# Kernel optimization log

Measured on AMD Instinct MI355X. Metric: run time of the kernel, lower is better.

Reference implementation:

```python
import jax, jax.numpy as jnp
import numpy as np

N_NODES = 100000
N_EDGES = 1600000
DIM = 32  # size_in


def setup_inputs() -> dict:
    key = jax.random.key(0)
    k = jax.random.split(key, 8)
    N, E, D = N_NODES, N_EDGES, DIM
    x = jax.random.normal(k[0], (N, 2 * D), dtype=jnp.float32)
    edge_index = jax.random.randint(k[1], (2, E), 0, N, dtype=jnp.int64)
    # Glorot-ish scaled weights (PyG GCNConv uses glorot init); biases zero.
    W1 = jax.random.normal(k[2], (2 * D, 2 * D), dtype=jnp.float32) * (1.0 / np.sqrt(2 * D))
    b1 = jnp.zeros((2 * D,), dtype=jnp.float32)
    W2 = jax.random.normal(k[3], (2 * D, D), dtype=jnp.float32) * (1.0 / np.sqrt(2 * D))
    b2 = jnp.zeros((D,), dtype=jnp.float32)
    W3 = jax.random.normal(k[4], (D, 1), dtype=jnp.float32) * (1.0 / np.sqrt(D))
    b3 = jnp.zeros((1,), dtype=jnp.float32)
    return {"x": x, "edge_index": edge_index, "W1": W1, "b1": b1,
            "W2": W2, "b2": b2, "W3": W3, "b3": b3}


def _gcn_norm(edge_index, num_nodes):
    # PyG gcn_norm with add_self_loops=True, edge_weight=1:
    # deg[i] = # incoming edges (incl. self loop); norm_e = deg[src]^-1/2 * deg[dst]^-1/2
    loop = jnp.arange(num_nodes, dtype=edge_index.dtype)
    src = jnp.concatenate([edge_index[0], loop])
    dst = jnp.concatenate([edge_index[1], loop])
    ones = jnp.ones(src.shape[0], dtype=jnp.float32)
    deg = jax.ops.segment_sum(ones, dst, num_segments=num_nodes)
    dis = jnp.where(deg > 0, jax.lax.rsqrt(deg), 0.0)
    norm = dis[src] * dis[dst]
    return src, dst, norm


def _gcn_conv(h, W, b, src, dst, norm, num_nodes):
    # linear transform first (PyG order), then normalized scatter-add aggregation
    h = h @ W  # [N, out]
    msg = h[src] * norm[:, None]  # gather over edges
    agg = jax.ops.segment_sum(msg, dst, num_segments=num_nodes)
    return agg + b


def reference(x, edge_index, W1, b1, W2, b2, W3, b3):
    N = x.shape[0]
    src, dst, norm = _gcn_norm(edge_index, N)
    out = jnp.tanh(_gcn_conv(x, W1, b1, src, dst, norm, N))
    out = jnp.tanh(_gcn_conv(out, W2, b2, src, dst, norm, N))
    out = _gcn_conv(out, W3, b3, src, dst, norm, N)
    return out
```

## Files before the change

### kernel.cpp

```cpp
#include <hip/hip_runtime.h>
#include <hip/hip_fp16.h>
#include <math.h>

static constexpr int NN = 100000;
static constexpr int NE = 1600000;
static constexpr int BUCK_SH = 5;
static constexpr int NBUK = NN >> BUCK_SH;
static constexpr int NCH = 256;
static constexpr int CH = NE / NCH;

__global__ __launch_bounds__(256)
void k_chist(const int* __restrict__ ei, int* __restrict__ H) {
  __shared__ int h[NBUK];
  for (int i = threadIdx.x; i < NBUK; i += 256) h[i] = 0;
  __syncthreads();
  int chunk = blockIdx.x;
  int start = chunk * CH;
  for (int e = start + threadIdx.x; e < start + CH; e += 256)
    atomicAdd(&h[ei[NE + e] >> BUCK_SH], 1);
  __syncthreads();
  int* Hc = H + chunk * NBUK;
  for (int i = threadIdx.x; i < NBUK; i += 256) Hc[i] = h[i];
}

__global__ void k_csum(int* __restrict__ H, int* __restrict__ tot) {
  int b = blockIdx.x * blockDim.x + threadIdx.x;
  if (b >= NBUK) return;
  int acc = 0;
#pragma unroll 4
  for (int c = 0; c < NCH; ++c) {
    int v = H[c * NBUK + b];
    H[c * NBUK + b] = acc;
    acc += v;
  }
  tot[b] = acc;
}

__global__ __launch_bounds__(1024)
void k_bscan(const int* __restrict__ tot, int* __restrict__ boff) {
  __shared__ int buf[1024];
  __shared__ int s_carry;
  int tid = threadIdx.x;
  if (tid == 0) s_carry = 0;
  __syncthreads();
  for (int base = 0; base < NBUK; base += 1024) {
    int i = base + tid;
    int v = (i < NBUK) ? tot[i] : 0;
    buf[tid] = v;
    __syncthreads();
#pragma unroll
    for (int off = 1; off < 1024; off <<= 1) {
      int t = (tid >= off) ? buf[tid - off] : 0;
      __syncthreads();
      buf[tid] += t;
      __syncthreads();
    }
    int excl = buf[tid] - v;
    int carry = s_carry;
    if (i < NBUK) boff[i] = carry + excl;
    __syncthreads();
    if (tid == 1023) s_carry = carry + buf[1023];
    __syncthreads();
  }
  if (tid == 0) boff[NBUK] = s_carry;
}

__global__ __launch_bounds__(1024)
void k_scat(const int* __restrict__ ei, const int* __restrict__ H,
            const int* __restrict__ boff, unsigned* __restrict__ se) {
  __shared__ int cur[NBUK];
  int chunk = blockIdx.x;
  const int* Hc = H + chunk * NBUK;
  for (int i = threadIdx.x; i < NBUK; i += 1024) cur[i] = boff[i] + Hc[i];
  __syncthreads();
  int start = chunk * CH;
  for (int e = start + threadIdx.x; e < start + CH; e += 1024) {
    int src = ei[e], dst = ei[NE + e];
    int pos = atomicAdd(&cur[dst >> BUCK_SH], 1);
    se[pos] = ((unsigned)(dst & 31) << 20) | (unsigned)src;
  }
}

__global__ __launch_bounds__(256)
void k_blocal(const unsigned* __restrict__ se, const int* __restrict__ boff,
              int* __restrict__ rowptr, float* __restrict__ dis, int* __restrict__ csr_src) {
  int b = blockIdx.x;
  int base = boff[b], end = boff[b + 1];
  __shared__ int cnt[32], off[32];
  int tid = threadIdx.x;
  if (tid < 32) cnt[tid] = 0;
  __syncthreads();
  for (int k = base + tid; k < end; k += 256)
    atomicAdd(&cnt[se[k] >> 20], 1);
  __syncthreads();
  if (tid == 0) {
    int acc = 0;
#pragma unroll
    for (int i = 0; i < 32; ++i) { off[i] = acc; acc += cnt[i]; }
  }
  __syncthreads();
  if (tid < 32) {
    int node = (b << BUCK_SH) + tid;
    rowptr[node] = base + off[tid];
    dis[node] = rsqrtf(1.0f + (float)cnt[tid]);
    cnt[tid] = 0;
  }
  if (b == 0 && tid == 64) rowptr[NN] = NE;
  __syncthreads();
  for (int k = base + tid; k < end; k += 256) {
    unsigned e = se[k];
    int dl = e >> 20;
    int pos = base + off[dl] + atomicAdd(&cnt[dl], 1);
    csr_src[pos] = (int)(e & 0xFFFFFu);
  }
}

__global__ __launch_bounds__(256)
void k_gemm64_h(const float* __restrict__ in, const float* __restrict__ W,
                const float* __restrict__ dis, __half* __restrict__ g) {
  __shared__ float rows[16 * 64];
  int c = threadIdx.x & 63;
  int wid = threadIdx.x >> 6;
  float Wc[64];
#pragma unroll
  for (int k = 0; k < 64; ++k) Wc[k] = W[k * 64 + c];
  int tiles = NN / 16;
  for (int t = blockIdx.x; t < tiles; t += gridDim.x) {
    int row0 = t * 16;
    __syncthreads();
    ((float4*)rows)[threadIdx.x] = ((const float4*)(in + (size_t)row0 * 64))[threadIdx.x];
    __syncthreads();
#pragma unroll
    for (int r = 0; r < 4; ++r) {
      const float* rp = rows + (wid * 4 + r) * 64;
      float acc = 0.f;
#pragma unroll
      for (int kc = 0; kc < 64; kc += 4) {
        float4 v = *(const float4*)(rp + kc);
        acc = fmaf(v.x, Wc[kc + 0], acc);
        acc = fmaf(v.y, Wc[kc + 1], acc);
        acc = fmaf(v.z, Wc[kc + 2], acc);
        acc = fmaf(v.w, Wc[kc + 3], acc);
      }
      int row = row0 + wid * 4 + r;
      g[row * 64 + c] = __float2half(acc * dis[row]);
    }
  }
}

__device__ __forceinline__ float fast_tanh(float x) {
  float e = __expf(2.0f * x);
  return 1.0f - 2.0f / (e + 1.0f);
}

__device__ __forceinline__ void upadd8(float4 r, float4& lo, float4& hi) {
  __half2* h = (__half2*)&r;
  float2 f0 = __half22float2(h[0]);
  float2 f1 = __half22float2(h[1]);
  float2 f2 = __half22float2(h[2]);
  float2 f3 = __half22float2(h[3]);
  lo.x += f0.x; lo.y += f0.y; lo.z += f1.x; lo.w += f1.y;
  hi.x += f2.x; hi.y += f2.y; hi.z += f3.x; hi.w += f3.y;
}

__global__ __launch_bounds__(256)
void k_agg64f(const int* __restrict__ rowptr, const int* __restrict__ csr_src,
              const __half* __restrict__ g, const float* __restrict__ dis,
              const float* __restrict__ b, const float* __restrict__ W2,
              __half* __restrict__ g2) {
  __shared__ float tile[4][8][68];
  int lane = threadIdx.x & 63;
  int wid = threadIdx.x >> 6;
  int grp = lane >> 3;
  int cl = lane & 7;
  int node = blockIdx.x * 32 + wid * 8 + grp;

  int c2 = lane & 31;
  int ksub = lane >> 5;
  float Wc[32];
#pragma unroll
  for (int k = 0; k < 32; ++k) Wc[k] = W2[(ksub * 32 + k) * 32 + c2];

  const char* base = (const char*)g;
  float4 l0 = {0,0,0,0}, h0 = {0,0,0,0}, l1 = {0,0,0,0}, h1 = {0,0,0,0};
  float4 l2 = {0,0,0,0}, h2 = {0,0,0,0}, l3 = {0,0,0,0}, h3 = {0,0,0,0};
  {
    float4 r = *(const float4*)(base + (size_t)node * 128 + cl * 16);
    upadd8(r, l0, h0);
  }
  int k = rowptr[node], end = rowptr[node + 1];
  for (; k + 4 <= end; k += 4) {
    int s0 = csr_src[k], s1 = csr_src[k + 1], s2 = csr_src[k + 2], s3 = csr_src[k + 3];
    float4 r0 = *(const float4*)(base + (size_t)s0 * 128 + cl * 16);
    float4 r1 = *(const float4*)(base + (size_t)s1 * 128 + cl * 16);
    float4 r2 = *(const float4*)(base + (size_t)s2 * 128 + cl * 16);
    float4 r3 = *(const float4*)(base + (size_t)s3 * 128 + cl * 16);
    upadd8(r0, l0, h0); upadd8(r1, l1, h1);
    upadd8(r2, l2, h2); upadd8(r3, l3, h3);
  }
  for (; k < end; ++k) {
    float4 r = *(const float4*)(base + (size_t)csr_src[k] * 128 + cl * 16);
    upadd8(r, l0, h0);
  }
  float d = dis[node];
  float4 blo = *(const float4*)(b + cl * 8);
  float4 bhi = *(const float4*)(b + cl * 8 + 4);
  float4 vl, vh;
  vl.x = ((l0.x + l1.x) + (l2.x + l3.x)) * d + blo.x;
  vl.y = ((l0.y + l1.y) + (l2.y + l3.y)) * d + blo.y;
  vl.z = ((l0.z + l1.z) + (l2.z + l3.z)) * d + blo.z;
  vl.w = ((l0.w + l1.w) + (l2.w + l3.w)) * d + blo.w;
  vh.x = ((h0.x + h1.x) + (h2.x + h3.x)) * d + bhi.x;
  vh.y = ((h0.y + h1.y) + (h2.y + h3.y)) * d + bhi.y;
  vh.z = ((h0.z + h1.z) + (h2.z + h3.z)) * d + bhi.z;
  vh.w = ((h0.w + h1.w) + (h2.w + h3.w)) * d + bhi.w;
  vl.x = fast_tanh(vl.x); vl.y = fast_tanh(vl.y);
  vl.z = fast_tanh(vl.z); vl.w = fast_tanh(vl.w);
  vh.x = fast_tanh(vh.x); vh.y = fast_tanh(vh.y);
  vh.z = fast_tanh(vh.z); vh.w = fast_tanh(vh.w);

  *(float4*)&tile[wid][grp][cl * 8] = vl;
  *(float4*)&tile[wid][grp][cl * 8 + 4] = vh;

  int rbase = blockIdx.x * 32 + wid * 8;
#pragma unroll
  for (int r = 0; r < 8; ++r) {
    const float* rp = &tile[wid][r][ksub * 32];
    float acc = 0.f;
#pragma unroll
    for (int kc = 0; kc < 32; kc += 4) {
      float4 v = *(const float4*)(rp + kc);
      acc = fmaf(v.x, Wc[kc + 0], acc);
      acc = fmaf(v.y, Wc[kc + 1], acc);
      acc = fmaf(v.z, Wc[kc + 2], acc);
      acc = fmaf(v.w, Wc[kc + 3], acc);
    }
    acc += __shfl_down(acc, 32);
    int row = rbase + r;
    if (ksub == 0) g2[row * 32 + c2] = __float2half(acc * dis[row]);
  }
}

__global__ __launch_bounds__(256)
void k_agg32v(const int* __restrict__ rowptr, const int* __restrict__ csr_src,
              const __half* __restrict__ g, const float* __restrict__ dis,
              const float* __restrict__ b, const float* __restrict__ W3,
              float* __restrict__ Af) {
  int lane = threadIdx.x & 63;
  int grp = lane >> 3;
  int cl = lane & 7;
  int node = blockIdx.x * 32 + (threadIdx.x >> 6) * 8 + grp;
  if (node >= NN) return;
  const char* base = (const char*)g;
  float4 a0 = {0,0,0,0}, a1 = {0,0,0,0}, a2 = {0,0,0,0}, a3 = {0,0,0,0};
  {
    float2 r = *(const float2*)(base + (size_t)node * 64 + cl * 8);
    __half2* h = (__half2*)&r;
    float2 f0 = __half22float2(h[0]), f1 = __half22float2(h[1]);
    a0.x += f0.x; a0.y += f0.y; a0.z += f1.x; a0.w += f1.y;
  }
  int k = rowptr[node], end = rowptr[node + 1];
  for (; k + 8 <= end; k += 8) {
    float2 r0 = *(const float2*)(base + (size_t)csr_src[k + 0] * 64 + cl * 8);
    float2 r1 = *(const float2*)(base + (size_t)csr_src[k + 1] * 64 + cl * 8);
    float2 r2 = *(const float2*)(base + (size_t)csr_src[k + 2] * 64 + cl * 8);
    float2 r3 = *(const float2*)(base + (size_t)csr_src[k + 3] * 64 + cl * 8);
    float2 r4 = *(const float2*)(base + (size_t)csr_src[k + 4] * 64 + cl * 8);
    float2 r5 = *(const float2*)(base + (size_t)csr_src[k + 5] * 64 + cl * 8);
    float2 r6 = *(const float2*)(base + (size_t)csr_src[k + 6] * 64 + cl * 8);
    float2 r7 = *(const float2*)(base + (size_t)csr_src[k + 7] * 64 + cl * 8);
    __half2* h; float2 f;
    h = (__half2*)&r0; f = __half22float2(h[0]); a0.x += f.x; a0.y += f.y;
    f = __half22float2(h[1]); a0.z += f.x; a0.w += f.y;
    h = (__half2*)&r1; f = __half22float2(h[0]); a1.x += f.x; a1.y += f.y;
    f = __half22float2(h[1]); a1.z += f.x; a1.w += f.y;
    h = (__half2*)&r2; f = __half22float2(h[0]); a2.x += f.x; a2.y += f.y;
    f = __half22float2(h[1]); a2.z += f.x; a2.w += f.y;
    h = (__half2*)&r3; f = __half22float2(h[0]); a3.x += f.x; a3.y += f.y;
    f = __half22float2(h[1]); a3.z += f.x; a3.w += f.y;
    h = (__half2*)&r4; f = __half22float2(h[0]); a0.x += f.x; a0.y += f.y;
    f = __half22float2(h[1]); a0.z += f.x; a0.w += f.y;
    h = (__half2*)&r5; f = __half22float2(h[0]); a1.x += f.x; a1.y += f.y;
    f = __half22float2(h[1]); a1.z += f.x; a1.w += f.y;
    h = (__half2*)&r6; f = __half22float2(h[0]); a2.x += f.x; a2.y += f.y;
    f = __half22float2(h[1]); a2.z += f.x; a2.w += f.y;
    h = (__half2*)&r7; f = __half22float2(h[0]); a3.x += f.x; a3.y += f.y;
    f = __half22float2(h[1]); a3.z += f.x; a3.w += f.y;
  }
  for (; k + 4 <= end; k += 4) {
    float2 r0 = *(const float2*)(base + (size_t)csr_src[k + 0] * 64 + cl * 8);
    float2 r1 = *(const float2*)(base + (size_t)csr_src[k + 1] * 64 + cl * 8);
    float2 r2 = *(const float2*)(base + (size_t)csr_src[k + 2] * 64 + cl * 8);
    float2 r3 = *(const float2*)(base + (size_t)csr_src[k + 3] * 64 + cl * 8);
    __half2* h; float2 f;
    h = (__half2*)&r0; f = __half22float2(h[0]); a0.x += f.x; a0.y += f.y;
    f = __half22float2(h[1]); a0.z += f.x; a0.w += f.y;
    h = (__half2*)&r1; f = __half22float2(h[0]); a1.x += f.x; a1.y += f.y;
    f = __half22float2(h[1]); a1.z += f.x; a1.w += f.y;
    h = (__half2*)&r2; f = __half22float2(h[0]); a2.x += f.x; a2.y += f.y;
    f = __half22float2(h[1]); a2.z += f.x; a2.w += f.y;
    h = (__half2*)&r3; f = __half22float2(h[0]); a3.x += f.x; a3.y += f.y;
    f = __half22float2(h[1]); a3.z += f.x; a3.w += f.y;
  }
  for (; k < end; ++k) {
    float2 r = *(const float2*)(base + (size_t)csr_src[k] * 64 + cl * 8);
    __half2* h = (__half2*)&r;
    float2 f0 = __half22float2(h[0]), f1 = __half22float2(h[1]);
    a0.x += f0.x; a0.y += f0.y; a0.z += f1.x; a0.w += f1.y;
  }
  float d = dis[node];
  float4 bb = *(const float4*)(b + cl * 4);
  float4 v;
  v.x = ((a0.x + a1.x) + (a2.x + a3.x)) * d + bb.x;
  v.y = ((a0.y + a1.y) + (a2.y + a3.y)) * d + bb.y;
  v.z = ((a0.z + a1.z) + (a2.z + a3.z)) * d + bb.z;
  v.w = ((a0.w + a1.w) + (a2.w + a3.w)) * d + bb.w;
  v.x = fast_tanh(v.x); v.y = fast_tanh(v.y);
  v.z = fast_tanh(v.z); v.w = fast_tanh(v.w);
  float4 w3 = *(const float4*)(W3 + cl * 4);
  float p = v.x * w3.x + v.y * w3.y + v.z * w3.z + v.w * w3.w;
  p += __shfl_xor(p, 1);
  p += __shfl_xor(p, 2);
  p += __shfl_xor(p, 4);
  if (cl == 0) Af[node] = p * d;
}

__global__ void k_agg1(const int* __restrict__ rowptr, const int* __restrict__ csr_src,
                       const float* __restrict__ g, const float* __restrict__ dis,
                       const float* __restrict__ b, float* __restrict__ out) {
  int node = blockIdx.x * blockDim.x + threadIdx.x;
  if (node >= NN) return;
  float a0 = g[node], a1 = 0.f, a2 = 0.f, a3 = 0.f;
  int beg = rowptr[node], end = rowptr[node + 1];
  int k = beg;
  for (; k + 4 <= end; k += 4) {
    float m0 = g[csr_src[k]], m1 = g[csr_src[k + 1]];
    float m2 = g[csr_src[k + 2]], m3 = g[csr_src[k + 3]];
    a0 += m0; a1 += m1; a2 += m2; a3 += m3;
  }
  for (; k < end; ++k) a0 += g[csr_src[k]];
  out[node] = ((a0 + a1) + (a2 + a3)) * dis[node] + b[0];
}

extern "C" void kernel_launch(void* const* d_in, const int* in_sizes, int n_in,
                              void* d_out, int out_size, void* d_ws, size_t ws_size,
                              hipStream_t stream) {
  const float* x  = (const float*)d_in[0];
  const int*   ei = (const int*)d_in[1];
  const float* W1 = (const float*)d_in[2];
  const float* b1 = (const float*)d_in[3];
  const float* W2 = (const float*)d_in[4];
  const float* b2 = (const float*)d_in[5];
  const float* W3 = (const float*)d_in[6];
  const float* b3 = (const float*)d_in[7];
  float* out = (float*)d_out;

  char* ws = (char*)d_ws;
  int*      H       = (int*)ws;      ws += (size_t)NCH * NBUK * 4;
  int*      tot     = (int*)ws;      ws += ((NBUK + 255)/256)*256 * 4;
  int*      boff    = (int*)ws;      ws += ((NBUK + 1 + 255)/256)*256 * 4;
  unsigned* se      = (unsigned*)ws; ws += (size_t)NE * 4;
  int*      rowptr  = (int*)ws;      ws += ((NN + 1 + 255)/256)*256 * 4;
  int*      csr_src = (int*)ws;      ws += (size_t)NE * 4;
  float*    dis     = (float*)ws;    ws += ((NN + 255)/256)*256 * 4;
  __half*   Ah      = (__half*)ws;   ws += (size_t)NN * 64 * 2;
  __half*   Ah2     = (__half*)ws;   ws += (size_t)NN * 32 * 2;
  float*    Af      = (float*)ws;    ws += (size_t)NN * 4;

  k_chist <<<NCH, 256, 0, stream>>>(ei, H);
  k_csum  <<<(NBUK + 255) / 256, 256, 0, stream>>>(H, tot);
  k_bscan <<<1, 1024, 0, stream>>>(tot, boff);
  k_scat  <<<NCH, 1024, 0, stream>>>(ei, H, boff, se);
  k_blocal<<<NBUK, 256, 0, stream>>>(se, boff, rowptr, dis, csr_src);

  k_gemm64_h<<<1250, 256, 0, stream>>>(x, W1, dis, Ah);
  k_agg64f<<<NN / 32, 256, 0, stream>>>(rowptr, csr_src, Ah, dis, b1, W2, Ah2);
  k_agg32v<<<NN / 32, 256, 0, stream>>>(rowptr, csr_src, Ah2, dis, b2, W3, Af);
  k_agg1<<<(NN + 255) / 256, 256, 0, stream>>>(rowptr, csr_src, Af, dis, b3, out);
}
```

Baseline: 252.0 us.

## Sort nodes by in-degree and process aggregation kernels in degree order

Builds a degree histogram in k_blocal, scans it, and scatters node ids into a degree-sorted permutation. The three aggregation kernels then process nodes through this permutation, so the 8 nodes sharing a wavefront have similar edge counts. This targets load imbalance and divergence inside a wavefront in the gather loops. The cost is two extra small kernels plus an atomic scatter, and output writes and row accesses are no longer contiguous in node order, which loses locality on rowptr, dis and the output stores.

```diff
diff --git a/kernel.cpp b/kernel.cpp
--- a/kernel.cpp
+++ b/kernel.cpp
@@ -10,8 +10,9 @@
 static constexpr int CH = NE / NCH;
 
 __global__ __launch_bounds__(256)
-void k_chist(const int* __restrict__ ei, int* __restrict__ H) {
+void k_chist(const int* __restrict__ ei, int* __restrict__ H, int* __restrict__ dh) {
   __shared__ int h[NBUK];
+  if (blockIdx.x == 0) dh[threadIdx.x] = 0;
   for (int i = threadIdx.x; i < NBUK; i += 256) h[i] = 0;
   __syncthreads();
   int chunk = blockIdx.x;
@@ -83,7 +84,8 @@
 
 __global__ __launch_bounds__(256)
 void k_blocal(const unsigned* __restrict__ se, const int* __restrict__ boff,
-              int* __restrict__ rowptr, float* __restrict__ dis, int* __restrict__ csr_src) {
+              int* __restrict__ rowptr, float* __restrict__ dis, int* __restrict__ csr_src,
+              int* __restrict__ deg, int* __restrict__ dh) {
   int b = blockIdx.x;
   int base = boff[b], end = boff[b + 1];
   __shared__ int cnt[32], off[32];
@@ -103,6 +105,9 @@
     int node = (b << BUCK_SH) + tid;
     rowptr[node] = base + off[tid];
     dis[node] = rsqrtf(1.0f + (float)cnt[tid]);
+    int d = cnt[tid] > 255 ? 255 : cnt[tid];
+    deg[node] = d;
+    atomicAdd(&dh[d], 1);
     cnt[tid] = 0;
   }
   if (b == 0 && tid == 64) rowptr[NN] = NE;
@@ -113,6 +118,31 @@
     int pos = base + off[dl] + atomicAdd(&cnt[dl], 1);
     csr_src[pos] = (int)(e & 0xFFFFFu);
   }
+}
+
+__global__ __launch_bounds__(256)
+void k_dscan(const int* __restrict__ dh, int* __restrict__ dcur) {
+  __shared__ int buf[256];
+  int tid = threadIdx.x;
+  int v = dh[tid];
+  buf[tid] = v;
+  __syncthreads();
+#pragma unroll
+  for (int off = 1; off < 256; off <<= 1) {
+    int t = (tid >= off) ? buf[tid - off] : 0;
+    __syncthreads();
+    buf[tid] += t;
+    __syncthreads();
+  }
+  dcur[tid] = buf[tid] - v;
+}
+
+__global__ void k_dperm(const int* __restrict__ deg, int* __restrict__ dcur,
+                        int* __restrict__ perm) {
+  int i = blockIdx.x * blockDim.x + threadIdx.x;
+  if (i >= NN) return;
+  int pos = atomicAdd(&dcur[deg[i]], 1);
+  perm[pos] = i;
 }
 
 __global__ __launch_bounds__(256)
@@ -167,13 +197,14 @@
 void k_agg64f(const int* __restrict__ rowptr, const int* __restrict__ csr_src,
               const __half* __restrict__ g, const float* __restrict__ dis,
               const float* __restrict__ b, const float* __restrict__ W2,
-              __half* __restrict__ g2) {
+              const int* __restrict__ perm, __half* __restrict__ g2) {
   __shared__ float tile[4][8][68];
   int lane = threadIdx.x & 63;
   int wid = threadIdx.x >> 6;
   int grp = lane >> 3;
   int cl = lane & 7;
-  int node = blockIdx.x * 32 + wid * 8 + grp;
+  int gid = blockIdx.x * 32 + wid * 8 + grp;
+  int node = perm[gid];
 
   int c2 = lane & 31;
   int ksub = lane >> 5;
@@ -236,8 +267,8 @@
       acc = fmaf(v.w, Wc[kc + 3], acc);
     }
     acc += __shfl_down(acc, 32);
-    int row = rbase + r;
-    if (ksub == 0) g2[row * 32 + c2] = __float2half(acc * dis[row]);
+    int noder = perm[rbase + r];
+    if (ksub == 0) g2[noder * 32 + c2] = __float2half(acc * dis[noder]);
   }
 }
 
@@ -245,12 +276,11 @@
 void k_agg32v(const int* __restrict__ rowptr, const int* __restrict__ csr_src,
               const __half* __restrict__ g, const float* __restrict__ dis,
               const float* __restrict__ b, const float* __restrict__ W3,
-              float* __restrict__ Af) {
+              const int* __restrict__ perm, float* __restrict__ Af) {
   int lane = threadIdx.x & 63;
   int grp = lane >> 3;
   int cl = lane & 7;
-  int node = blockIdx.x * 32 + (threadIdx.x >> 6) * 8 + grp;
-  if (node >= NN) return;
+  int node = perm[blockIdx.x * 32 + (threadIdx.x >> 6) * 8 + grp];
   const char* base = (const char*)g;
   float4 a0 = {0,0,0,0}, a1 = {0,0,0,0}, a2 = {0,0,0,0}, a3 = {0,0,0,0};
   {
@@ -327,9 +357,11 @@
 
 __global__ void k_agg1(const int* __restrict__ rowptr, const int* __restrict__ csr_src,
                        const float* __restrict__ g, const float* __restrict__ dis,
-                       const float* __restrict__ b, float* __restrict__ out) {
-  int node = blockIdx.x * blockDim.x + threadIdx.x;
-  if (node >= NN) return;
+                       const float* __restrict__ b, const int* __restrict__ perm,
+                       float* __restrict__ out) {
+  int i = blockIdx.x * blockDim.x + threadIdx.x;
+  if (i >= NN) return;
+  int node = perm[i];
   float a0 = g[node], a1 = 0.f, a2 = 0.f, a3 = 0.f;
   int beg = rowptr[node], end = rowptr[node + 1];
   int k = beg;
@@ -363,18 +395,24 @@
   int*      rowptr  = (int*)ws;      ws += ((NN + 1 + 255)/256)*256 * 4;
   int*      csr_src = (int*)ws;      ws += (size_t)NE * 4;
   float*    dis     = (float*)ws;    ws += ((NN + 255)/256)*256 * 4;
+  int*      deg     = (int*)ws;      ws += ((NN + 255)/256)*256 * 4;
+  int*      perm    = (int*)ws;      ws += ((NN + 255)/256)*256 * 4;
+  int*      dh      = (int*)ws;      ws += 256 * 4;
+  int*      dcur    = (int*)ws;      ws += 256 * 4;
   __half*   Ah      = (__half*)ws;   ws += (size_t)NN * 64 * 2;
   __half*   Ah2     = (__half*)ws;   ws += (size_t)NN * 32 * 2;
   float*    Af      = (float*)ws;    ws += (size_t)NN * 4;
 
-  k_chist <<<NCH, 256, 0, stream>>>(ei, H);
+  k_chist <<<NCH, 256, 0, stream>>>(ei, H, dh);
   k_csum  <<<(NBUK + 255) / 256, 256, 0, stream>>>(H, tot);
   k_bscan <<<1, 1024, 0, stream>>>(tot, boff);
   k_scat  <<<NCH, 1024, 0, stream>>>(ei, H, boff, se);
-  k_blocal<<<NBUK, 256, 0, stream>>>(se, boff, rowptr, dis, csr_src);
+  k_blocal<<<NBUK, 256, 0, stream>>>(se, boff, rowptr, dis, csr_src, deg, dh);
+  k_dscan <<<1, 256, 0, stream>>>(dh, dcur);
+  k_dperm <<<(NN + 255) / 256, 256, 0, stream>>>(deg, dcur, perm);
 
   k_gemm64_h<<<1250, 256, 0, stream>>>(x, W1, dis, Ah);
-  k_agg64f<<<NN / 32, 256, 0, stream>>>(rowptr, csr_src, Ah, dis, b1, W2, Ah2);
-  k_agg32v<<<NN / 32, 256, 0, stream>>>(rowptr, csr_src, Ah2, dis, b2, W3, Af);
-  k_agg1<<<(NN + 255) / 256, 256, 0, stream>>>(rowptr, csr_src, Af, dis, b3, out);
-}
+  k_agg64f<<<NN / 32, 256, 0, stream>>>(rowptr, csr_src, Ah, dis, b1, W2, perm, Ah2);
+  k_agg32v<<<NN / 32, 256, 0, stream>>>(rowptr, csr_src, Ah2, dis, b2, W3, perm, Af);
+  k_agg1<<<(NN + 255) / 256, 256, 0, stream>>>(rowptr, csr_src, Af, dis, b3, perm, out);
+}
```

Measured after the change: 789.2 us. +213.2%, slower.
